# Performance work log

Measured on AMD Instinct MI355X. Metric: run time of the kernel, lower is better.

The kernel has to match this reference:

```python
import jax, jax.numpy as jnp
import numpy as np

B, L, D = 4, 4096, 1024
C = 8.0  # fixed exponent scale from the module (self.c = 8)


def setup_inputs() -> dict:
    key = jax.random.key(0)
    ks = jax.random.split(key, 4)
    std = 1.0 / np.sqrt(D)  # kaiming normal, fan_in, linear
    x = jax.random.normal(ks[0], (B, L, D), dtype=jnp.float32)
    Wa = jax.random.normal(ks[1], (D, D), dtype=jnp.float32) * std
    Wx = jax.random.normal(ks[2], (D, D), dtype=jnp.float32) * std
    ba = jnp.zeros((D,), dtype=jnp.float32)
    bx = jnp.zeros((D,), dtype=jnp.float32)
    # lmbd ~ U(0.9, 0.999)
    lmbd = 0.9 + 0.099 * jax.random.uniform(ks[3], (D,), dtype=jnp.float32)
    return {"x": x, "Wa": Wa, "Wx": Wx, "ba": ba, "bx": bx, "lmbd": lmbd}


def reference(x, Wa, Wx, ba, bx, lmbd):
    # a = sigmoid(lmbd) computed once at init in the original module
    log_a = jnp.log(jax.nn.sigmoid(lmbd))  # [D], negative
    # Batched projections upfront (F.linear uses W @ x^T, i.e. x @ W.T)
    r = jax.nn.sigmoid(jnp.einsum('bld,hd->blh', x, Wa) + ba)  # recurrence gate
    i = jax.nn.sigmoid(jnp.einsum('bld,hd->blh', x, Wx) + bx)  # input gate
    a_t = jnp.exp(C * r * log_a)                 # a ** (c * r), [B,L,D]
    b_t = jnp.sqrt(1.0 - a_t * a_t) * (i * x)    # [B,L,D]
    # Linear recurrence h_t = a_t * h_{t-1} + b_t, h_0 = 0
    def step(h, ab):
        at, bt = ab
        h = at * h + bt
        return h, h
    h0 = jnp.zeros((x.shape[0], x.shape[2]), dtype=x.dtype)
    _, y = jax.lax.scan(step, h0, (jnp.swapaxes(a_t, 0, 1), jnp.swapaxes(b_t, 0, 1)))
    return jnp.swapaxes(y, 0, 1)  # [B, L, D]
```

## Files before the change

kernel.cpp:

```cpp
#include <hip/hip_runtime.h>
#include <stdint.h>
#include <math.h>


#define D_DIM 1024
#define L_DIM 4096
#define B_DIM 4
#define M_DIM (B_DIM * L_DIM)
#define N_DIM (2 * D_DIM)
#define K_DIM D_DIM
#define NC 32
#define CL (L_DIM / NC)
#define L2E 1.4426950408889634f

typedef __attribute__((ext_vector_type(8))) short short8;
typedef __attribute__((ext_vector_type(4))) short short4v;
typedef __attribute__((ext_vector_type(4))) float float4v;

__device__ __forceinline__ unsigned short f2bf(float f) {
  unsigned u = __float_as_uint(f);
  u += 0x7fffu + ((u >> 16) & 1u);
  return (unsigned short)(u >> 16);
}
__device__ __forceinline__ float bf2f(unsigned short h) {
  return __uint_as_float((unsigned)h << 16);
}
__device__ __forceinline__ short f2h(float f) {
  _Float16 h = (_Float16)f;
  return __builtin_bit_cast(short, h);
}

#define NX16 (M_DIM * K_DIM / 8)
#define NW16 (N_DIM * K_DIM / 8)

__global__ void pack_all(const float* __restrict__ x, const float* __restrict__ Wa,
                         const float* __restrict__ Wx, short* __restrict__ Xs,
                         short* __restrict__ Ws) {
  int t = blockIdx.x * 256 + threadIdx.x;
  const float* src;
  short8* dst;
  int u;
  if (t < NX16) {
    u = t; src = x; dst = (short8*)Xs;
  } else {
    u = t - NX16;
    if (u >= NW16) return;
    dst = (short8*)Ws;
    int row = ((u >> 11) << 4) | (u & 15);
    src = (row < D_DIM) ? Wa : (Wx - (size_t)D_DIM * K_DIM);
  }
  int r  = u & 15;
  int kc = (u >> 4) & 3;
  int k0 = (u >> 6) & 31;
  int R  = u >> 11;
  int m = R * 16 + r;
  int k = (k0 * 4 + kc) * 8;
  const float4v* s4 = (const float4v*)(src + (size_t)m * 1024 + k);
  float4v v0 = s4[0], v1 = s4[1];
  short8 o;
  o[0] = (short)f2bf(v0.x); o[1] = (short)f2bf(v0.y);
  o[2] = (short)f2bf(v0.z); o[3] = (short)f2bf(v0.w);
  o[4] = (short)f2bf(v1.x); o[5] = (short)f2bf(v1.y);
  o[6] = (short)f2bf(v1.z); o[7] = (short)f2bf(v1.w);
  dst[u] = o;
}

__global__ __launch_bounds__(256, 4) void gemm_gates(
    const short* __restrict__ Xs,
    const short* __restrict__ Ws,
    const float* __restrict__ xf,
    const float* __restrict__ ba,
    const float* __restrict__ bx,
    const float* __restrict__ lmbd,
    short* __restrict__ e_out,
    unsigned short* __restrict__ g_out)
{
  __shared__ __align__(16) char smem[17664];

  const int tile_n = blockIdx.x * 128;
  const int tile_m = blockIdx.y * 128;
  const int tid  = threadIdx.x;
  const int wave = tid >> 6;
  const int lane = tid & 63;
  const int row16 = lane & 15;
  const int quad  = lane >> 4;
  const int wave_m = (wave & 1) * 64;
  const int wave_n = (wave >> 1) * 64;

  short* As = (short*)smem;
  short* Bs = (short*)(smem + 8192);
  char* AsB = smem;
  char* BsB = smem + 8192;

  float4v acc[4][4] = {};

  for (int kk = 0; kk < 32; ++kk) {
#pragma unroll
    for (int p = 0; p < 2; ++p) {
      const int G = p * 4 + wave;
      const size_t RgA = (size_t)((tile_m >> 4) + G);
      const size_t RgB = (size_t)((tile_n >> 4) + G);
      __builtin_amdgcn_global_load_lds(
          (const __attribute__((address_space(1))) void*)(Xs + ((RgA * 32 + kk) * 64 + lane) * 8),
          (__attribute__((address_space(3))) void*)(AsB + G * 1024),
          16, 0, 0);
      __builtin_amdgcn_global_load_lds(
          (const __attribute__((address_space(1))) void*)(Ws + ((RgB * 32 + kk) * 64 + lane) * 8),
          (__attribute__((address_space(3))) void*)(BsB + G * 1024),
          16, 0, 0);
    }
    __syncthreads();

    short8 af[4], bfr[4];
#pragma unroll
    for (int i = 0; i < 4; ++i)
      af[i] = *(const short8*)&As[((wave & 1) * 4 + i) * 512 + lane * 8];
#pragma unroll
    for (int i = 0; i < 4; ++i)
      bfr[i] = *(const short8*)&Bs[((wave >> 1) * 4 + i) * 512 + lane * 8];

#pragma unroll
    for (int mi = 0; mi < 4; ++mi)
#pragma unroll
      for (int ni = 0; ni < 4; ++ni)
        acc[mi][ni] = __builtin_amdgcn_mfma_f32_16x16x32_bf16(af[mi], bfr[ni], acc[mi][ni], 0, 0, 0);
    __syncthreads();
  }

  float* Ts = (float*)smem + (size_t)wave * (16 * 68);
  const int colg = (lane & 15) * 4;
  const int rrow = lane >> 4;
  const bool is_a = (tile_n < D_DIM);
  const int ch0 = (is_a ? tile_n : tile_n - D_DIM) + wave_n + colg;

  float4v bias4, la84;
  if (is_a) {
    bias4 = *(const float4v*)(ba + ch0);
    float4v lm4 = *(const float4v*)(lmbd + ch0);
#pragma unroll
    for (int k = 0; k < 4; ++k)
      la84[k] = -8.0f * __builtin_amdgcn_logf(1.0f + __builtin_amdgcn_exp2f(-lm4[k] * L2E));
  } else {
    bias4 = *(const float4v*)(bx + ch0);
  }

#pragma unroll
  for (int mi = 0; mi < 4; ++mi) {
#pragma unroll
    for (int ni = 0; ni < 4; ++ni)
#pragma unroll
      for (int r = 0; r < 4; ++r)
        Ts[(quad * 4 + r) * 68 + ni * 16 + row16] = acc[mi][ni][r];
#pragma unroll
    for (int j = 0; j < 4; ++j) {
      int lr = j * 4 + rrow;
      float4v z = *(const float4v*)&Ts[lr * 68 + colg];
      size_t gm = (size_t)(tile_m + wave_m + mi * 16 + lr);
      short4v o;
      if (is_a) {
#pragma unroll
        for (int k = 0; k < 4; ++k) {
          float s = __builtin_amdgcn_rcpf(1.0f + __builtin_amdgcn_exp2f(-(z[k] + bias4[k]) * L2E));
          o[k] = f2h(s * la84[k]);
        }
        *(short4v*)(e_out + gm * D_DIM + ch0) = o;
      } else {
        float4v xv = *(const float4v*)(xf + gm * D_DIM + ch0);
#pragma unroll
        for (int k = 0; k < 4; ++k) {
          float s = __builtin_amdgcn_rcpf(1.0f + __builtin_amdgcn_exp2f(-(z[k] + bias4[k]) * L2E));
          o[k] = (short)f2bf(s * xv[k]);
        }
        *(short4v*)((short*)g_out + gm * D_DIM + ch0) = o;
      }
    }
  }
}

__global__ void scan_phase1(const short* __restrict__ e, const unsigned short* __restrict__ g,
                            float* __restrict__ P, float* __restrict__ Q) {
  int d = blockIdx.x * 256 + threadIdx.x;
  int c = blockIdx.y;
  int b = blockIdx.z;
  const size_t base = ((size_t)(b * L_DIM + c * CL)) * D_DIM + d;
  float Pv = 1.0f, Qv = 0.0f;
#pragma unroll 4
  for (int t = 0; t < CL; ++t) {
    float ev = (float)__builtin_bit_cast(_Float16, e[base + (size_t)t * D_DIM]);
    float at = __builtin_amdgcn_exp2f(ev);
    float gv = bf2f(g[base + (size_t)t * D_DIM]);
    float bt = sqrtf(fmaxf(1.0f - at * at, 0.0f)) * gv;
    Qv = fmaf(at, Qv, bt);
    Pv *= at;
  }
  int idx = (b * NC + c) * D_DIM + d;
  P[idx] = Pv;
  Q[idx] = Qv;
}

__global__ void scan_phase3(const short* __restrict__ e, const unsigned short* __restrict__ g,
                            const float* __restrict__ P, const float* __restrict__ Q,
                            float* __restrict__ y) {
  int d = blockIdx.x * 256 + threadIdx.x;
  int c = blockIdx.y;
  int b = blockIdx.z;
  float h = 0.0f;
#pragma unroll 4
  for (int cc = 0; cc < c; ++cc) {
    int idx = (b * NC + cc) * D_DIM + d;
    h = fmaf(P[idx], h, Q[idx]);
  }
  const size_t base = ((size_t)(b * L_DIM + c * CL)) * D_DIM + d;
#pragma unroll 4
  for (int t = 0; t < CL; ++t) {
    float ev = (float)__builtin_bit_cast(_Float16, e[base + (size_t)t * D_DIM]);
    float at = __builtin_amdgcn_exp2f(ev);
    float gv = bf2f(g[base + (size_t)t * D_DIM]);
    float bt = sqrtf(fmaxf(1.0f - at * at, 0.0f)) * gv;
    h = fmaf(at, h, bt);
    y[base + (size_t)t * D_DIM] = h;
  }
}

extern "C" void kernel_launch(void* const* d_in, const int* in_sizes, int n_in,
                              void* d_out, int out_size, void* d_ws, size_t ws_size,
                              hipStream_t stream) {
  const float* x    = (const float*)d_in[0];
  const float* Wa   = (const float*)d_in[1];
  const float* Wx   = (const float*)d_in[2];
  const float* ba   = (const float*)d_in[3];
  const float* bx   = (const float*)d_in[4];
  const float* lmbd = (const float*)d_in[5];
  float* y = (float*)d_out;

  char* ws = (char*)d_ws;
  short* Xs             = (short*)ws;
  short* Wsz            = (short*)(ws + 33554432);
  short* e_buf          = (short*)(ws + 37748736);
  unsigned short* g_buf = (unsigned short*)(ws + 71303168);
  float* P              = (float*)(ws + 104857600);
  float* Q              = (float*)(ws + 105381888);

  pack_all<<<(NX16 + NW16) / 256, 256, 0, stream>>>(x, Wa, Wx, Xs, Wsz);

  dim3 gg(N_DIM / 128, M_DIM / 128);
  gemm_gates<<<gg, 256, 0, stream>>>(Xs, Wsz, x, ba, bx, lmbd, e_buf, g_buf);

  dim3 sg(D_DIM / 256, NC, B_DIM);
  scan_phase1<<<sg, 256, 0, stream>>>(e_buf, g_buf, P, Q);
  scan_phase3<<<sg, 256, 0, stream>>>(e_buf, g_buf, P, Q, y);
}
```

Baseline: 252.4 us.

## Rewrite gate GEMM with 256x256 tiles, double-buffered LDS and XCD-aware block swizzle

The gate GEMM moves from 128x128 tiles with 4 waves and a single synchronous LDS buffer to 256x256 tiles with 8 waves and two 64KB LDS buffers. Loads for the next k-step are interleaved with the MFMA work on the current one, paced by explicit vmcnt waits and raised wave priority around the MFMAs. The pack kernel's layout changes to match the new tile and k-chunk ordering, and block IDs are remapped so each XCD works on a contiguous group of tiles. The aim is to hide global-load latency and improve operand reuse and L2 locality, at the cost of one block per CU and heavy LDS and register use.

```diff
diff --git a/kernel.cpp b/kernel.cpp
--- a/kernel.cpp
+++ b/kernel.cpp
@@ -40,21 +40,19 @@
   const float* src;
   short8* dst;
   int u;
+  int m;
   if (t < NX16) {
-    u = t; src = x; dst = (short8*)Xs;
+    u = t; dst = (short8*)Xs;
+    m = (u >> 15) * 256 + ((u >> 10) & 1) * 128 + ((u >> 6) & 7) * 16 + (u & 15);
+    src = x;
   } else {
     u = t - NX16;
     if (u >= NW16) return;
     dst = (short8*)Ws;
-    int row = ((u >> 11) << 4) | (u & 15);
-    src = (row < D_DIM) ? Wa : (Wx - (size_t)D_DIM * K_DIM);
-  }
-  int r  = u & 15;
-  int kc = (u >> 4) & 3;
-  int k0 = (u >> 6) & 31;
-  int R  = u >> 11;
-  int m = R * 16 + r;
-  int k = (k0 * 4 + kc) * 8;
+    m = (u >> 15) * 256 + ((u >> 10) & 1) * 128 + ((u >> 6) & 7) * 16 + (u & 15);
+    src = (m < D_DIM) ? Wa : (Wx - (size_t)D_DIM * K_DIM);
+  }
+  int k = ((u >> 11) & 15) * 64 + ((u >> 9) & 1) * 32 + ((u >> 4) & 3) * 8;
   const float4v* s4 = (const float4v*)(src + (size_t)m * 1024 + k);
   float4v v0 = s4[0], v1 = s4[1];
   short8 o;
@@ -65,7 +63,7 @@
   dst[u] = o;
 }
 
-__global__ __launch_bounds__(256, 4) void gemm_gates(
+__global__ __launch_bounds__(512, 1) void gemm_gates(
     const short* __restrict__ Xs,
     const short* __restrict__ Ws,
     const float* __restrict__ xf,
@@ -75,63 +73,128 @@
     short* __restrict__ e_out,
     unsigned short* __restrict__ g_out)
 {
-  __shared__ __align__(16) char smem[17664];
-
-  const int tile_n = blockIdx.x * 128;
-  const int tile_m = blockIdx.y * 128;
+  __shared__ __align__(16) char smem[131072];
+
+  const int bid = blockIdx.y * 8 + blockIdx.x;
+  const int nb  = (bid & 7) * 64 + (bid >> 3);
+  const int tile_n = (nb & 7) * 256;
+  const int tile_m = (nb >> 3) * 256;
   const int tid  = threadIdx.x;
   const int wave = tid >> 6;
   const int lane = tid & 63;
+  const int wm = wave >> 2;
+  const int wn = wave & 3;
+  const size_t mS = (size_t)(tile_m >> 8);
+  const size_t nS = (size_t)(tile_n >> 8);
+
+  float4v acc[8][4] = {};
+
+#define STAGE(Xsel, Hs, kss, ktN, bufN)                                        \
+  do {                                                                         \
+    const size_t bg_ = ((((Xsel ? nS : mS) * 16 + (size_t)(ktN)) * 2 +         \
+                        (size_t)(Hs)) * 2 + (size_t)(kss)) * 512;              \
+    const short* sp_ = (Xsel ? Ws : Xs) + (bg_ + (size_t)tid) * 8;             \
+    __builtin_amdgcn_global_load_lds(                                          \
+        (const __attribute__((address_space(1))) void*)sp_,                    \
+        (__attribute__((address_space(3))) void*)(smem + (bufN) * 65536 +      \
+            (((Xsel) * 2 + (Hs)) * 2 + (kss)) * 8192 + wave * 1024),           \
+        16, 0, 0);                                                             \
+  } while (0)
+
+#pragma unroll
+  for (int X = 0; X < 2; ++X)
+#pragma unroll
+    for (int H = 0; H < 2; ++H)
+#pragma unroll
+      for (int ks = 0; ks < 2; ++ks)
+        STAGE(X, H, ks, 0, 0);
+  asm volatile("s_waitcnt vmcnt(0)" ::: "memory");
+  __builtin_amdgcn_sched_barrier(0);
+  __builtin_amdgcn_s_barrier();
+
+  const int aBase = (wm * 2) * 8192;
+  const int bBase = ((2 + (wn >> 1)) * 2) * 8192;
+  const int bGrp  = (wn & 1) * 4;
+
+  for (int kt = 0; kt < 16; ++kt) {
+    const int cur = kt & 1;
+    const int nxt = cur ^ 1;
+    const bool stg = (kt < 15);
+    const char* buf = smem + cur * 65536;
+    short8 af[4], bf[4];
+
+    if (stg) { STAGE(0, 0, 0, kt + 1, nxt); STAGE(0, 1, 0, kt + 1, nxt); }
+    if (stg) asm volatile("s_waitcnt vmcnt(6)" ::: "memory");
+    else     asm volatile("s_waitcnt vmcnt(4)" ::: "memory");
+    __builtin_amdgcn_sched_barrier(0);
+    __builtin_amdgcn_s_barrier();
+#pragma unroll
+    for (int i = 0; i < 4; ++i)
+      af[i] = *(const short8*)(buf + aBase + i * 1024 + lane * 16);
+#pragma unroll
+    for (int i = 0; i < 4; ++i)
+      bf[i] = *(const short8*)(buf + bBase + (bGrp + i) * 1024 + lane * 16);
+    __builtin_amdgcn_s_setprio(1);
+#pragma unroll
+    for (int i = 0; i < 4; ++i)
+#pragma unroll
+      for (int ni = 0; ni < 4; ++ni)
+        acc[i][ni] = __builtin_amdgcn_mfma_f32_16x16x32_bf16(af[i], bf[ni], acc[i][ni], 0, 0, 0);
+    __builtin_amdgcn_s_setprio(0);
+
+    if (stg) { STAGE(1, 0, 0, kt + 1, nxt); STAGE(1, 1, 0, kt + 1, nxt); }
+#pragma unroll
+    for (int i = 0; i < 4; ++i)
+      af[i] = *(const short8*)(buf + aBase + (4 + i) * 1024 + lane * 16);
+    __builtin_amdgcn_s_setprio(1);
+#pragma unroll
+    for (int i = 0; i < 4; ++i)
+#pragma unroll
+      for (int ni = 0; ni < 4; ++ni)
+        acc[4 + i][ni] = __builtin_amdgcn_mfma_f32_16x16x32_bf16(af[i], bf[ni], acc[4 + i][ni], 0, 0, 0);
+    __builtin_amdgcn_s_setprio(0);
+
+    if (stg) { STAGE(0, 0, 1, kt + 1, nxt); STAGE(0, 1, 1, kt + 1, nxt); }
+    if (stg) asm volatile("s_waitcnt vmcnt(6)" ::: "memory");
+    else     asm volatile("s_waitcnt vmcnt(0)" ::: "memory");
+    __builtin_amdgcn_sched_barrier(0);
+    __builtin_amdgcn_s_barrier();
+#pragma unroll
+    for (int i = 0; i < 4; ++i)
+      af[i] = *(const short8*)(buf + aBase + 8192 + i * 1024 + lane * 16);
+#pragma unroll
+    for (int i = 0; i < 4; ++i)
+      bf[i] = *(const short8*)(buf + bBase + 8192 + (bGrp + i) * 1024 + lane * 16);
+    __builtin_amdgcn_s_setprio(1);
+#pragma unroll
+    for (int i = 0; i < 4; ++i)
+#pragma unroll
+      for (int ni = 0; ni < 4; ++ni)
+        acc[i][ni] = __builtin_amdgcn_mfma_f32_16x16x32_bf16(af[i], bf[ni], acc[i][ni], 0, 0, 0);
+    __builtin_amdgcn_s_setprio(0);
+
+    if (stg) { STAGE(1, 0, 1, kt + 1, nxt); STAGE(1, 1, 1, kt + 1, nxt); }
+#pragma unroll
+    for (int i = 0; i < 4; ++i)
+      af[i] = *(const short8*)(buf + aBase + 8192 + (4 + i) * 1024 + lane * 16);
+    __builtin_amdgcn_s_setprio(1);
+#pragma unroll
+    for (int i = 0; i < 4; ++i)
+#pragma unroll
+      for (int ni = 0; ni < 4; ++ni)
+        acc[4 + i][ni] = __builtin_amdgcn_mfma_f32_16x16x32_bf16(af[i], bf[ni], acc[4 + i][ni], 0, 0, 0);
+    __builtin_amdgcn_s_setprio(0);
+    __builtin_amdgcn_s_barrier();
+  }
+#undef STAGE
+
+  float* Ts = (float*)smem + (size_t)wave * (16 * 68);
   const int row16 = lane & 15;
   const int quad  = lane >> 4;
-  const int wave_m = (wave & 1) * 64;
-  const int wave_n = (wave >> 1) * 64;
-
-  short* As = (short*)smem;
-  short* Bs = (short*)(smem + 8192);
-  char* AsB = smem;
-  char* BsB = smem + 8192;
-
-  float4v acc[4][4] = {};
-
-  for (int kk = 0; kk < 32; ++kk) {
-#pragma unroll
-    for (int p = 0; p < 2; ++p) {
-      const int G = p * 4 + wave;
-      const size_t RgA = (size_t)((tile_m >> 4) + G);
-      const size_t RgB = (size_t)((tile_n >> 4) + G);
-      __builtin_amdgcn_global_load_lds(
-          (const __attribute__((address_space(1))) void*)(Xs + ((RgA * 32 + kk) * 64 + lane) * 8),
-          (__attribute__((address_space(3))) void*)(AsB + G * 1024),
-          16, 0, 0);
-      __builtin_amdgcn_global_load_lds(
-          (const __attribute__((address_space(1))) void*)(Ws + ((RgB * 32 + kk) * 64 + lane) * 8),
-          (__attribute__((address_space(3))) void*)(BsB + G * 1024),
-          16, 0, 0);
-    }
-    __syncthreads();
-
-    short8 af[4], bfr[4];
-#pragma unroll
-    for (int i = 0; i < 4; ++i)
-      af[i] = *(const short8*)&As[((wave & 1) * 4 + i) * 512 + lane * 8];
-#pragma unroll
-    for (int i = 0; i < 4; ++i)
-      bfr[i] = *(const short8*)&Bs[((wave >> 1) * 4 + i) * 512 + lane * 8];
-
-#pragma unroll
-    for (int mi = 0; mi < 4; ++mi)
-#pragma unroll
-      for (int ni = 0; ni < 4; ++ni)
-        acc[mi][ni] = __builtin_amdgcn_mfma_f32_16x16x32_bf16(af[mi], bfr[ni], acc[mi][ni], 0, 0, 0);
-    __syncthreads();
-  }
-
-  float* Ts = (float*)smem + (size_t)wave * (16 * 68);
   const int colg = (lane & 15) * 4;
   const int rrow = lane >> 4;
   const bool is_a = (tile_n < D_DIM);
-  const int ch0 = (is_a ? tile_n : tile_n - D_DIM) + wave_n + colg;
+  const int ch0 = (is_a ? tile_n : tile_n - D_DIM) + wn * 64 + colg;
 
   float4v bias4, la84;
   if (is_a) {
@@ -145,7 +208,7 @@
   }
 
 #pragma unroll
-  for (int mi = 0; mi < 4; ++mi) {
+  for (int mi = 0; mi < 8; ++mi) {
 #pragma unroll
     for (int ni = 0; ni < 4; ++ni)
 #pragma unroll
@@ -155,7 +218,7 @@
     for (int j = 0; j < 4; ++j) {
       int lr = j * 4 + rrow;
       float4v z = *(const float4v*)&Ts[lr * 68 + colg];
-      size_t gm = (size_t)(tile_m + wave_m + mi * 16 + lr);
+      size_t gm = (size_t)(tile_m + wm * 128 + mi * 16 + lr);
       short4v o;
       if (is_a) {
 #pragma unroll
@@ -243,8 +306,8 @@
 
   pack_all<<<(NX16 + NW16) / 256, 256, 0, stream>>>(x, Wa, Wx, Xs, Wsz);
 
-  dim3 gg(N_DIM / 128, M_DIM / 128);
-  gemm_gates<<<gg, 256, 0, stream>>>(Xs, Wsz, x, ba, bx, lmbd, e_buf, g_buf);
+  dim3 gg(N_DIM / 256, M_DIM / 256);
+  gemm_gates<<<gg, 512, 0, stream>>>(Xs, Wsz, x, ba, bx, lmbd, e_buf, g_buf);
 
   dim3 sg(D_DIM / 256, NC, B_DIM);
   scan_phase1<<<sg, 256, 0, stream>>>(e_buf, g_buf, P, Q);
```

After: 252.1 us. About the same (-0.1%).
